# Performance work log

Hardware: AMD Instinct MI355X
Metric: run time of the kernel (lower is better)

The kernel has to match this reference:

```python
import jax, jax.numpy as jnp
import numpy as np

B, S, D, E, K = 4, 4096, 2048, 64, 2


def setup_inputs() -> dict:
    key = jax.random.key(0)
    k1, k2 = jax.random.split(key)
    hidden_states = jax.random.normal(k1, (B, S, D), dtype=jnp.float32)
    gate_weight = jax.random.normal(k2, (E, D), dtype=jnp.float32) * 0.02
    return {"hidden_states": hidden_states, "gate_weight": gate_weight}


def reference(hidden_states, gate_weight):
    b, s, d = hidden_states.shape
    e = gate_weight.shape[0]
    n = b * s
    x = hidden_states.reshape(n, d)
    logits = x @ gate_weight.T                                  # [N, E]
    # Original reassigns gate_logits = softmax(gate_logits) in fp32.
    probs = jax.nn.softmax(logits.astype(jnp.float32), axis=-1)  # [N, E]

    top_v, top_i = jax.lax.top_k(probs, K)                       # [N, K]
    top_k_gates = top_v  # normalize_gate_prob_before_dropping=False

    oh = jax.nn.one_hot(top_i, e, dtype=probs.dtype)             # [N, K, E]
    gates = jnp.einsum('nke,nk->ne', oh, top_k_gates)            # scatter of top-k gates

    # Auxiliary losses (training path, use_aux_loss=True)
    gates_mean = gates.mean(axis=0)                              # [E]
    selection_mean = oh.sum(axis=(0, 1)) / n                     # [E]
    load_balancing_loss = (gates_mean * selection_mean).sum() * e
    # NOTE: original computes z-loss on the softmaxed probs (gate_logits was overwritten)
    router_z_loss = (jax.nn.logsumexp(probs, axis=-1) ** 2).mean()

    # torch scatter_ with index [B,S,1,1] only ever writes slot k=0.
    dispatch0 = oh.sum(axis=1).reshape(b, s, e)                  # 1.0 at top-k experts
    combine0 = gates.reshape(b, s, e)
    pad = ((0, 0), (0, 0), (0, 0), (0, K - 1))
    dispatch_tensor = jnp.pad(dispatch0[..., None], pad)         # [B,S,E,K]
    combine_tensor = jnp.pad(combine0[..., None], pad)           # [B,S,E,K]

    return dispatch_tensor, combine_tensor, load_balancing_loss, router_z_loss
```

## Files before the change

kernel.cpp:

```cpp
#include <hip/hip_runtime.h>
#include <hip/hip_bf16.h>
#include <cstddef>

namespace {
constexpr int kD = 2048;
constexpr int kE = 64;
constexpr int kN = 16384;
constexpr size_t kDispatchFloats = (size_t)kN * kE * 2;
}

typedef short short8_t __attribute__((ext_vector_type(8)));
typedef float f32x4 __attribute__((ext_vector_type(4)));

__global__ void zero_ws_kernel(float* __restrict__ ws) {
  ws[threadIdx.x] = 0.0f;
}

__device__ __forceinline__ void split3(float f, unsigned short& s1,
                                       unsigned short& s2, unsigned short& s3) {
  __hip_bfloat16 h1 = __float2bfloat16(f);
  float r1 = (f - __bfloat162float(h1)) * 256.0f;
  __hip_bfloat16 h2 = __float2bfloat16(r1);
  float r2 = (r1 - __bfloat162float(h2)) * 256.0f;
  __hip_bfloat16 h3 = __float2bfloat16(r2);
  s1 = __builtin_bit_cast(unsigned short, h1);
  s2 = __builtin_bit_cast(unsigned short, h2);
  s3 = __builtin_bit_cast(unsigned short, h3);
}

__global__ __launch_bounds__(256)
void logits_kernel(const float* __restrict__ x, const float* __restrict__ W,
                   float* __restrict__ out) {
  __shared__ unsigned short xs[3][64][64];
  __shared__ unsigned short wsh[3][64][64];

  const int tid  = threadIdx.x;
  const int tile = blockIdx.x & 255;
  const int dq   = blockIdx.x >> 8;

  const int row = tid >> 2;
  const int seg = tid & 3;
  const float4* __restrict__ bx = reinterpret_cast<const float4*>(x) +
      ((size_t)(tile * 64 + row)) * 512 + dq * 128 + seg * 4;
  const float4* __restrict__ bw = reinterpret_cast<const float4*>(W) +
      (size_t)row * 512 + dq * 128 + seg * 4;

  const int lane = tid & 63;
  const int wv   = __builtin_amdgcn_readfirstlane(tid >> 6);
  const int wr   = wv >> 1;
  const int wc   = wv & 1;
  const int lrow = lane & 15;
  const int lk   = lane >> 4;

  f32x4 acc0[2][2], acc1[2][2], acc2[2][2];
  const f32x4 z4 = {0.0f, 0.0f, 0.0f, 0.0f};
#pragma unroll
  for (int a = 0; a < 2; ++a)
#pragma unroll
    for (int b = 0; b < 2; ++b) { acc0[a][b] = z4; acc1[a][b] = z4; acc2[a][b] = z4; }

  for (int c = 0; c < 8; ++c) {
    __syncthreads();
    float4 vx[4], vw[4];
#pragma unroll
    for (int j = 0; j < 4; ++j) vx[j] = bx[c * 16 + j];
#pragma unroll
    for (int j = 0; j < 4; ++j) vw[j] = bw[c * 16 + j];

    {
      short8_t o1[2], o2[2], o3[2];
#pragma unroll
      for (int j = 0; j < 4; ++j) {
        const float4 v = vx[j];
        const int ch = j >> 1, b0 = (j & 1) * 4;
        unsigned short s1, s2, s3;
        split3(v.x, s1, s2, s3); o1[ch][b0+0]=(short)s1; o2[ch][b0+0]=(short)s2; o3[ch][b0+0]=(short)s3;
        split3(v.y, s1, s2, s3); o1[ch][b0+1]=(short)s1; o2[ch][b0+1]=(short)s2; o3[ch][b0+1]=(short)s3;
        split3(v.z, s1, s2, s3); o1[ch][b0+2]=(short)s1; o2[ch][b0+2]=(short)s2; o3[ch][b0+2]=(short)s3;
        split3(v.w, s1, s2, s3); o1[ch][b0+3]=(short)s1; o2[ch][b0+3]=(short)s2; o3[ch][b0+3]=(short)s3;
      }
#pragma unroll
      for (int ch = 0; ch < 2; ++ch) {
        const int col = (seg * 2 + ch) ^ (row & 7);
        *reinterpret_cast<short8_t*>(&xs[0][row][col * 8]) = o1[ch];
        *reinterpret_cast<short8_t*>(&xs[1][row][col * 8]) = o2[ch];
        *reinterpret_cast<short8_t*>(&xs[2][row][col * 8]) = o3[ch];
      }
    }
    {
      short8_t o1[2], o2[2], o3[2];
#pragma unroll
      for (int j = 0; j < 4; ++j) {
        const float4 v = vw[j];
        const int ch = j >> 1, b0 = (j & 1) * 4;
        unsigned short s1, s2, s3;
        split3(v.x, s1, s2, s3); o1[ch][b0+0]=(short)s1; o2[ch][b0+0]=(short)s2; o3[ch][b0+0]=(short)s3;
        split3(v.y, s1, s2, s3); o1[ch][b0+1]=(short)s1; o2[ch][b0+1]=(short)s2; o3[ch][b0+1]=(short)s3;
        split3(v.z, s1, s2, s3); o1[ch][b0+2]=(short)s1; o2[ch][b0+2]=(short)s2; o3[ch][b0+2]=(short)s3;
        split3(v.w, s1, s2, s3); o1[ch][b0+3]=(short)s1; o2[ch][b0+3]=(short)s2; o3[ch][b0+3]=(short)s3;
      }
#pragma unroll
      for (int ch = 0; ch < 2; ++ch) {
        const int col = (seg * 2 + ch) ^ (row & 7);
        *reinterpret_cast<short8_t*>(&wsh[0][row][col * 8]) = o1[ch];
        *reinterpret_cast<short8_t*>(&wsh[1][row][col * 8]) = o2[ch];
        *reinterpret_cast<short8_t*>(&wsh[2][row][col * 8]) = o3[ch];
      }
    }
    __syncthreads();

#pragma unroll
    for (int ks = 0; ks < 2; ++ks) {
      const int kc = ks * 4 + lk;
      short8_t a1[2], a2[2], a3[2], b1[2], b2[2], b3[2];
#pragma unroll
      for (int mt = 0; mt < 2; ++mt) {
        const int r = wr * 32 + mt * 16 + lrow;
        const int cw = (kc ^ (r & 7)) * 8;
        a1[mt] = *reinterpret_cast<const short8_t*>(&xs[0][r][cw]);
        a2[mt] = *reinterpret_cast<const short8_t*>(&xs[1][r][cw]);
        a3[mt] = *reinterpret_cast<const short8_t*>(&xs[2][r][cw]);
      }
#pragma unroll
      for (int nt = 0; nt < 2; ++nt) {
        const int e = wc * 32 + nt * 16 + lrow;
        const int cw = (kc ^ (e & 7)) * 8;
        b1[nt] = *reinterpret_cast<const short8_t*>(&wsh[0][e][cw]);
        b2[nt] = *reinterpret_cast<const short8_t*>(&wsh[1][e][cw]);
        b3[nt] = *reinterpret_cast<const short8_t*>(&wsh[2][e][cw]);
      }
#pragma unroll
      for (int mt = 0; mt < 2; ++mt)
#pragma unroll
        for (int nt = 0; nt < 2; ++nt) {
          acc0[mt][nt] = __builtin_amdgcn_mfma_f32_16x16x32_bf16(a1[mt], b1[nt], acc0[mt][nt], 0, 0, 0);
          acc1[mt][nt] = __builtin_amdgcn_mfma_f32_16x16x32_bf16(a1[mt], b2[nt], acc1[mt][nt], 0, 0, 0);
          acc1[mt][nt] = __builtin_amdgcn_mfma_f32_16x16x32_bf16(a2[mt], b1[nt], acc1[mt][nt], 0, 0, 0);
          acc2[mt][nt] = __builtin_amdgcn_mfma_f32_16x16x32_bf16(a1[mt], b3[nt], acc2[mt][nt], 0, 0, 0);
          acc2[mt][nt] = __builtin_amdgcn_mfma_f32_16x16x32_bf16(a3[mt], b1[nt], acc2[mt][nt], 0, 0, 0);
          acc2[mt][nt] = __builtin_amdgcn_mfma_f32_16x16x32_bf16(a2[mt], b2[nt], acc2[mt][nt], 0, 0, 0);
        }
    }
  }

  const float k8 = 1.0f / 256.0f, k16 = 1.0f / 65536.0f;
  float* __restrict__ base = out + ((dq < 2) ? (size_t)0 : kDispatchFloats);
#pragma unroll
  for (int mt = 0; mt < 2; ++mt)
#pragma unroll
    for (int r = 0; r < 4; ++r) {
      const int trow = wr * 32 + mt * 16 + lk * 4 + r;
      const size_t n = (size_t)tile * 64 + trow;
      float* __restrict__ dst =
          base + n * 128 + (dq & 1) * 64 + wc * 32 + lrow;
#pragma unroll
      for (int nt = 0; nt < 2; ++nt) {
        dst[nt * 16] = acc0[mt][nt][r] + acc1[mt][nt][r] * k8 + acc2[mt][nt][r] * k16;
      }
    }
}

__global__ __launch_bounds__(256)
void gate_kernel(float* __restrict__ out, float* __restrict__ ws) {
  __shared__ float lg[64][65];
  __shared__ int ti0[64], ti1[64];
  __shared__ float tv0[64], tv1[64], tz2[64];
  const int tid  = threadIdx.x;
  const int tile = blockIdx.x;

  float* __restrict__ outd = out + (size_t)tile * 8192;
  float* __restrict__ outc = out + kDispatchFloats + (size_t)tile * 8192;
  const float4* __restrict__ d4 = reinterpret_cast<const float4*>(outd);
  const float4* __restrict__ c4 = reinterpret_cast<const float4*>(outc);

  const int tq = tid >> 4, q = tid & 15;
#pragma unroll
  for (int k = 0; k < 4; ++k) {
    const int t = k * 16 + tq;
    const float4 a = d4[t * 32 + q];
    const float4 b = d4[t * 32 + 16 + q];
    const float4 c = c4[t * 32 + q];
    const float4 d = c4[t * 32 + 16 + q];
    lg[t][q * 4 + 0] = a.x + b.x + c.x + d.x;
    lg[t][q * 4 + 1] = a.y + b.y + c.y + d.y;
    lg[t][q * 4 + 2] = a.z + b.z + c.z + d.z;
    lg[t][q * 4 + 3] = a.w + b.w + c.w + d.w;
  }
  __syncthreads();

  if (tid < 64) {
    float v0 = -INFINITY, v1 = -INFINITY;
    int i0 = 0, i1 = 0;
    for (int e = 0; e < kE; ++e) {
      const float l = lg[tid][e];
      if (l > v0) { v1 = v0; i1 = i0; v0 = l; i0 = e; }
      else if (l > v1) { v1 = l; i1 = e; }
    }
    const float m = v0;
    float s = 0.0f;
    for (int e = 0; e < kE; ++e) s += __expf(lg[tid][e] - m);
    const float rs = 1.0f / s;
    float zexp = 0.0f;
    for (int e = 0; e < kE; ++e) zexp += __expf(__expf(lg[tid][e] - m) * rs);
    const float z = logf(zexp);
    ti0[tid] = i0; ti1[tid] = i1;
    tv0[tid] = rs;
    tv1[tid] = __expf(v1 - m) * rs;
    tz2[tid] = z * z;
  }
  __syncthreads();

  if (tid < kE) {
    float g = 0.0f, cnt = 0.0f;
    for (int t = 0; t < 64; ++t) {
      if (ti0[t] == tid) { g += tv0[t]; cnt += 1.0f; }
      if (ti1[t] == tid) { g += tv1[t]; cnt += 1.0f; }
    }
    atomicAdd(&ws[tid], g);
    atomicAdd(&ws[kE + tid], cnt);
    float z2 = tz2[tid];
    for (int off = 32; off; off >>= 1) z2 += __shfl_down(z2, off);
    if (tid == 0) atomicAdd(&ws[2 * kE], z2);
  }

  {
    const int t = tid >> 2, sub = tid & 3;
    const int i0 = ti0[t], i1 = ti1[t];
    const float v0 = tv0[t], v1 = tv1[t];
    float4* __restrict__ dp = reinterpret_cast<float4*>(outd) + t * 32;
    float4* __restrict__ cp = reinterpret_cast<float4*>(outc) + t * 32;
#pragma unroll
    for (int j = 0; j < 8; ++j) {
      const int qq = sub * 8 + j;
      const int e0 = qq * 2, e1 = qq * 2 + 1;
      const float d0v = (e0 == i0 || e0 == i1) ? 1.0f : 0.0f;
      const float d1v = (e1 == i0 || e1 == i1) ? 1.0f : 0.0f;
      const float c0 = (e0 == i0) ? v0 : ((e0 == i1) ? v1 : 0.0f);
      const float c1 = (e1 == i0) ? v0 : ((e1 == i1) ? v1 : 0.0f);
      dp[qq] = make_float4(d0v, 0.0f, d1v, 0.0f);
      cp[qq] = make_float4(c0, 0.0f, c1, 0.0f);
    }
  }
}

__global__ void finalize_kernel(const float* __restrict__ ws,
                                float* __restrict__ out) {
  const int e = threadIdx.x;
  float prod = ws[e] * ws[kE + e];
  for (int off = 32; off; off >>= 1) prod += __shfl_down(prod, off);
  if (e == 0) {
    const size_t base = kDispatchFloats * 2;
    const float invN = 1.0f / (float)kN;
    out[base]     = prod * ((float)kE * invN * invN);
    out[base + 1] = ws[2 * kE] * invN;
  }
}

extern "C" void kernel_launch(void* const* d_in, const int* in_sizes, int n_in,
                              void* d_out, int out_size, void* d_ws,
                              size_t ws_size, hipStream_t stream) {
  const float* x = (const float*)d_in[0];
  const float* W = (const float*)d_in[1];
  float* out = (float*)d_out;
  float* ws = (float*)d_ws;

  zero_ws_kernel<<<1, 256, 0, stream>>>(ws);
  logits_kernel<<<1024, 256, 0, stream>>>(x, W, out);
  gate_kernel<<<256, 256, 0, stream>>>(out, ws);
  finalize_kernel<<<1, kE, 0, stream>>>(ws, out);
}
```

Baseline: 75.23 us.

## Fuse logits GEMM and gating into one kernel with in-block split-K

Merges the logits GEMM and the gate/top-k kernel into a single 512-thread kernel per 64-token tile. Two wave groups each cover half of D and reduce into a shared-memory logits tile with LDS atomics. Each wave now prefetches the next chunk into registers while the MFMAs run. This removes the global round trip of the partial logits through the output buffer and one kernel launch. The cost is only 256 blocks instead of 1024, which lowers parallelism and occupancy, and larger LDS use per block.

```diff
diff --git a/kernel.cpp b/kernel.cpp
--- a/kernel.cpp
+++ b/kernel.cpp
@@ -28,30 +28,60 @@
   s3 = __builtin_bit_cast(unsigned short, h3);
 }
 
-__global__ __launch_bounds__(256)
-void logits_kernel(const float* __restrict__ x, const float* __restrict__ W,
-                   float* __restrict__ out) {
-  __shared__ unsigned short xs[3][64][64];
-  __shared__ unsigned short wsh[3][64][64];
+__device__ __forceinline__ void conv_store(const float4* v,
+                                           unsigned short (*dst)[64][64],
+                                           int srow, int seg) {
+  short8_t o1[2], o2[2], o3[2];
+#pragma unroll
+  for (int j = 0; j < 4; ++j) {
+    const float4 f = v[j];
+    const int ch = j >> 1, b0 = (j & 1) * 4;
+    unsigned short s1, s2, s3;
+    split3(f.x, s1, s2, s3); o1[ch][b0+0]=(short)s1; o2[ch][b0+0]=(short)s2; o3[ch][b0+0]=(short)s3;
+    split3(f.y, s1, s2, s3); o1[ch][b0+1]=(short)s1; o2[ch][b0+1]=(short)s2; o3[ch][b0+1]=(short)s3;
+    split3(f.z, s1, s2, s3); o1[ch][b0+2]=(short)s1; o2[ch][b0+2]=(short)s2; o3[ch][b0+2]=(short)s3;
+    split3(f.w, s1, s2, s3); o1[ch][b0+3]=(short)s1; o2[ch][b0+3]=(short)s2; o3[ch][b0+3]=(short)s3;
+  }
+#pragma unroll
+  for (int ch = 0; ch < 2; ++ch) {
+    const int col = (seg * 2 + ch) ^ (srow & 7);
+    *reinterpret_cast<short8_t*>(&dst[0][srow][col * 8]) = o1[ch];
+    *reinterpret_cast<short8_t*>(&dst[1][srow][col * 8]) = o2[ch];
+    *reinterpret_cast<short8_t*>(&dst[2][srow][col * 8]) = o3[ch];
+  }
+}
+
+__global__ __launch_bounds__(512)
+void moe_fused_kernel(const float* __restrict__ x, const float* __restrict__ W,
+                      float* __restrict__ out, float* __restrict__ ws) {
+  __shared__ unsigned short xs[2][3][64][64];
+  __shared__ unsigned short wh[2][3][64][64];
+  __shared__ float lg[64][65];
+  __shared__ int ti0[64], ti1[64];
+  __shared__ float tv0[64], tv1[64], tz2[64];
 
   const int tid  = threadIdx.x;
-  const int tile = blockIdx.x & 255;
-  const int dq   = blockIdx.x >> 8;
-
-  const int row = tid >> 2;
-  const int seg = tid & 3;
-  const float4* __restrict__ bx = reinterpret_cast<const float4*>(x) +
-      ((size_t)(tile * 64 + row)) * 512 + dq * 128 + seg * 4;
-  const float4* __restrict__ bw = reinterpret_cast<const float4*>(W) +
-      (size_t)row * 512 + dq * 128 + seg * 4;
-
   const int lane = tid & 63;
   const int wv   = __builtin_amdgcn_readfirstlane(tid >> 6);
-  const int wr   = wv >> 1;
+  const int kh   = wv >> 2;
+  const int wr   = (wv >> 1) & 1;
   const int wc   = wv & 1;
+  const int tile = blockIdx.x;
   const int lrow = lane & 15;
   const int lk   = lane >> 4;
 
+  const int h = tid & 255;
+  const int srow = h >> 2, seg = h & 3;
+  const float4* __restrict__ bx = reinterpret_cast<const float4*>(x) +
+      ((size_t)tile * 64 + srow) * 512 + kh * 256 + seg * 4;
+  const float4* __restrict__ bw = reinterpret_cast<const float4*>(W) +
+      (size_t)srow * 512 + kh * 256 + seg * 4;
+
+  {
+    float* lgf = &lg[0][0];
+    for (int i = tid; i < 64 * 65; i += 512) lgf[i] = 0.0f;
+  }
+
   f32x4 acc0[2][2], acc1[2][2], acc2[2][2];
   const f32x4 z4 = {0.0f, 0.0f, 0.0f, 0.0f};
 #pragma unroll
@@ -59,56 +89,22 @@
 #pragma unroll
     for (int b = 0; b < 2; ++b) { acc0[a][b] = z4; acc1[a][b] = z4; acc2[a][b] = z4; }
 
-  for (int c = 0; c < 8; ++c) {
-    __syncthreads();
-    float4 vx[4], vw[4];
-#pragma unroll
-    for (int j = 0; j < 4; ++j) vx[j] = bx[c * 16 + j];
-#pragma unroll
-    for (int j = 0; j < 4; ++j) vw[j] = bw[c * 16 + j];
-
-    {
-      short8_t o1[2], o2[2], o3[2];
-#pragma unroll
-      for (int j = 0; j < 4; ++j) {
-        const float4 v = vx[j];
-        const int ch = j >> 1, b0 = (j & 1) * 4;
-        unsigned short s1, s2, s3;
-        split3(v.x, s1, s2, s3); o1[ch][b0+0]=(short)s1; o2[ch][b0+0]=(short)s2; o3[ch][b0+0]=(short)s3;
-        split3(v.y, s1, s2, s3); o1[ch][b0+1]=(short)s1; o2[ch][b0+1]=(short)s2; o3[ch][b0+1]=(short)s3;
-        split3(v.z, s1, s2, s3); o1[ch][b0+2]=(short)s1; o2[ch][b0+2]=(short)s2; o3[ch][b0+2]=(short)s3;
-        split3(v.w, s1, s2, s3); o1[ch][b0+3]=(short)s1; o2[ch][b0+3]=(short)s2; o3[ch][b0+3]=(short)s3;
-      }
-#pragma unroll
-      for (int ch = 0; ch < 2; ++ch) {
-        const int col = (seg * 2 + ch) ^ (row & 7);
-        *reinterpret_cast<short8_t*>(&xs[0][row][col * 8]) = o1[ch];
-        *reinterpret_cast<short8_t*>(&xs[1][row][col * 8]) = o2[ch];
-        *reinterpret_cast<short8_t*>(&xs[2][row][col * 8]) = o3[ch];
-      }
-    }
-    {
-      short8_t o1[2], o2[2], o3[2];
-#pragma unroll
-      for (int j = 0; j < 4; ++j) {
-        const float4 v = vw[j];
-        const int ch = j >> 1, b0 = (j & 1) * 4;
-        unsigned short s1, s2, s3;
-        split3(v.x, s1, s2, s3); o1[ch][b0+0]=(short)s1; o2[ch][b0+0]=(short)s2; o3[ch][b0+0]=(short)s3;
-        split3(v.y, s1, s2, s3); o1[ch][b0+1]=(short)s1; o2[ch][b0+1]=(short)s2; o3[ch][b0+1]=(short)s3;
-        split3(v.z, s1, s2, s3); o1[ch][b0+2]=(short)s1; o2[ch][b0+2]=(short)s2; o3[ch][b0+2]=(short)s3;
-        split3(v.w, s1, s2, s3); o1[ch][b0+3]=(short)s1; o2[ch][b0+3]=(short)s2; o3[ch][b0+3]=(short)s3;
-      }
-#pragma unroll
-      for (int ch = 0; ch < 2; ++ch) {
-        const int col = (seg * 2 + ch) ^ (row & 7);
-        *reinterpret_cast<short8_t*>(&wsh[0][row][col * 8]) = o1[ch];
-        *reinterpret_cast<short8_t*>(&wsh[1][row][col * 8]) = o2[ch];
-        *reinterpret_cast<short8_t*>(&wsh[2][row][col * 8]) = o3[ch];
-      }
-    }
-    __syncthreads();
-
+  float4 vx[4], vw[4];
+#pragma unroll
+  for (int j = 0; j < 4; ++j) vx[j] = bx[j];
+#pragma unroll
+  for (int j = 0; j < 4; ++j) vw[j] = bw[j];
+  conv_store(vx, xs[kh], srow, seg);
+  conv_store(vw, wh[kh], srow, seg);
+  __syncthreads();
+
+  for (int c = 0; c < 16; ++c) {
+    if (c < 15) {
+#pragma unroll
+      for (int j = 0; j < 4; ++j) vx[j] = bx[(c + 1) * 16 + j];
+#pragma unroll
+      for (int j = 0; j < 4; ++j) vw[j] = bw[(c + 1) * 16 + j];
+    }
 #pragma unroll
     for (int ks = 0; ks < 2; ++ks) {
       const int kc = ks * 4 + lk;
@@ -117,17 +113,17 @@
       for (int mt = 0; mt < 2; ++mt) {
         const int r = wr * 32 + mt * 16 + lrow;
         const int cw = (kc ^ (r & 7)) * 8;
-        a1[mt] = *reinterpret_cast<const short8_t*>(&xs[0][r][cw]);
-        a2[mt] = *reinterpret_cast<const short8_t*>(&xs[1][r][cw]);
-        a3[mt] = *reinterpret_cast<const short8_t*>(&xs[2][r][cw]);
+        a1[mt] = *reinterpret_cast<const short8_t*>(&xs[kh][0][r][cw]);
+        a2[mt] = *reinterpret_cast<const short8_t*>(&xs[kh][1][r][cw]);
+        a3[mt] = *reinterpret_cast<const short8_t*>(&xs[kh][2][r][cw]);
       }
 #pragma unroll
       for (int nt = 0; nt < 2; ++nt) {
         const int e = wc * 32 + nt * 16 + lrow;
         const int cw = (kc ^ (e & 7)) * 8;
-        b1[nt] = *reinterpret_cast<const short8_t*>(&wsh[0][e][cw]);
-        b2[nt] = *reinterpret_cast<const short8_t*>(&wsh[1][e][cw]);
-        b3[nt] = *reinterpret_cast<const short8_t*>(&wsh[2][e][cw]);
+        b1[nt] = *reinterpret_cast<const short8_t*>(&wh[kh][0][e][cw]);
+        b2[nt] = *reinterpret_cast<const short8_t*>(&wh[kh][1][e][cw]);
+        b3[nt] = *reinterpret_cast<const short8_t*>(&wh[kh][2][e][cw]);
       }
 #pragma unroll
       for (int mt = 0; mt < 2; ++mt)
@@ -141,51 +137,24 @@
           acc2[mt][nt] = __builtin_amdgcn_mfma_f32_16x16x32_bf16(a2[mt], b2[nt], acc2[mt][nt], 0, 0, 0);
         }
     }
+    __syncthreads();
+    if (c < 15) {
+      conv_store(vx, xs[kh], srow, seg);
+      conv_store(vw, wh[kh], srow, seg);
+    }
+    __syncthreads();
   }
 
   const float k8 = 1.0f / 256.0f, k16 = 1.0f / 65536.0f;
-  float* __restrict__ base = out + ((dq < 2) ? (size_t)0 : kDispatchFloats);
 #pragma unroll
   for (int mt = 0; mt < 2; ++mt)
 #pragma unroll
-    for (int r = 0; r < 4; ++r) {
-      const int trow = wr * 32 + mt * 16 + lk * 4 + r;
-      const size_t n = (size_t)tile * 64 + trow;
-      float* __restrict__ dst =
-          base + n * 128 + (dq & 1) * 64 + wc * 32 + lrow;
-#pragma unroll
-      for (int nt = 0; nt < 2; ++nt) {
-        dst[nt * 16] = acc0[mt][nt][r] + acc1[mt][nt][r] * k8 + acc2[mt][nt][r] * k16;
+    for (int nt = 0; nt < 2; ++nt)
+#pragma unroll
+      for (int r = 0; r < 4; ++r) {
+        const float v = acc0[mt][nt][r] + acc1[mt][nt][r] * k8 + acc2[mt][nt][r] * k16;
+        atomicAdd(&lg[wr * 32 + mt * 16 + lk * 4 + r][wc * 32 + nt * 16 + lrow], v);
       }
-    }
-}
-
-__global__ __launch_bounds__(256)
-void gate_kernel(float* __restrict__ out, float* __restrict__ ws) {
-  __shared__ float lg[64][65];
-  __shared__ int ti0[64], ti1[64];
-  __shared__ float tv0[64], tv1[64], tz2[64];
-  const int tid  = threadIdx.x;
-  const int tile = blockIdx.x;
-
-  float* __restrict__ outd = out + (size_t)tile * 8192;
-  float* __restrict__ outc = out + kDispatchFloats + (size_t)tile * 8192;
-  const float4* __restrict__ d4 = reinterpret_cast<const float4*>(outd);
-  const float4* __restrict__ c4 = reinterpret_cast<const float4*>(outc);
-
-  const int tq = tid >> 4, q = tid & 15;
-#pragma unroll
-  for (int k = 0; k < 4; ++k) {
-    const int t = k * 16 + tq;
-    const float4 a = d4[t * 32 + q];
-    const float4 b = d4[t * 32 + 16 + q];
-    const float4 c = c4[t * 32 + q];
-    const float4 d = c4[t * 32 + 16 + q];
-    lg[t][q * 4 + 0] = a.x + b.x + c.x + d.x;
-    lg[t][q * 4 + 1] = a.y + b.y + c.y + d.y;
-    lg[t][q * 4 + 2] = a.z + b.z + c.z + d.z;
-    lg[t][q * 4 + 3] = a.w + b.w + c.w + d.w;
-  }
   __syncthreads();
 
   if (tid < 64) {
@@ -224,14 +193,16 @@
   }
 
   {
-    const int t = tid >> 2, sub = tid & 3;
+    const int t = tid >> 3, sub = tid & 7;
     const int i0 = ti0[t], i1 = ti1[t];
     const float v0 = tv0[t], v1 = tv1[t];
-    float4* __restrict__ dp = reinterpret_cast<float4*>(outd) + t * 32;
-    float4* __restrict__ cp = reinterpret_cast<float4*>(outc) + t * 32;
-#pragma unroll
-    for (int j = 0; j < 8; ++j) {
-      const int qq = sub * 8 + j;
+    float4* __restrict__ dp =
+        reinterpret_cast<float4*>(out) + ((size_t)tile * 64 + t) * 32;
+    float4* __restrict__ cp =
+        reinterpret_cast<float4*>(out) + (size_t)kN * 32 + ((size_t)tile * 64 + t) * 32;
+#pragma unroll
+    for (int j = 0; j < 4; ++j) {
+      const int qq = sub * 4 + j;
       const int e0 = qq * 2, e1 = qq * 2 + 1;
       const float d0v = (e0 == i0 || e0 == i1) ? 1.0f : 0.0f;
       const float d1v = (e1 == i0 || e1 == i1) ? 1.0f : 0.0f;
@@ -265,7 +236,6 @@
   float* ws = (float*)d_ws;
 
   zero_ws_kernel<<<1, 256, 0, stream>>>(ws);
-  logits_kernel<<<1024, 256, 0, stream>>>(x, W, out);
-  gate_kernel<<<256, 256, 0, stream>>>(out, ws);
+  moe_fused_kernel<<<256, 512, 0, stream>>>(x, W, out, ws);
   finalize_kernel<<<1, kE, 0, stream>>>(ws, out);
 }
```

Result: slower. 84.14 us (+11.8%).

## Pre-split gate weights into bf16 triples once and prefetch next x chunk

Applied to the files above, without the earlier changes.

A new kernel converts W into three bf16 planes in workspace once per call, instead of every logits block redoing the split. Logits blocks now read the B fragments for the MFMAs directly from global memory (L2-resident) and drop the W shared-memory tile. The x loads for the next chunk are issued before the MFMA loop, overlapping global latency with compute. The cost is an extra kernel launch, and uncoalesced-ish global fragment loads that stand in for LDS reads.

```diff
diff --git a/kernel.cpp b/kernel.cpp
--- a/kernel.cpp
+++ b/kernel.cpp
@@ -7,6 +7,7 @@
 constexpr int kE = 64;
 constexpr int kN = 16384;
 constexpr size_t kDispatchFloats = (size_t)kN * kE * 2;
+constexpr size_t kWsplitOff = 1024;
 }
 
 typedef short short8_t __attribute__((ext_vector_type(8)));
@@ -29,29 +30,68 @@
 }
 
 __global__ __launch_bounds__(256)
-void logits_kernel(const float* __restrict__ x, const float* __restrict__ W,
+void split_w_kernel(const float* __restrict__ W, unsigned short* __restrict__ wsp) {
+  const int i = blockIdx.x * 256 + threadIdx.x;
+  const float4* src = reinterpret_cast<const float4*>(W) + i * 2;
+  const float4 v0 = src[0], v1 = src[1];
+  short8_t o1, o2, o3;
+  unsigned short s1, s2, s3;
+  split3(v0.x, s1, s2, s3); o1[0]=(short)s1; o2[0]=(short)s2; o3[0]=(short)s3;
+  split3(v0.y, s1, s2, s3); o1[1]=(short)s1; o2[1]=(short)s2; o3[1]=(short)s3;
+  split3(v0.z, s1, s2, s3); o1[2]=(short)s1; o2[2]=(short)s2; o3[2]=(short)s3;
+  split3(v0.w, s1, s2, s3); o1[3]=(short)s1; o2[3]=(short)s2; o3[3]=(short)s3;
+  split3(v1.x, s1, s2, s3); o1[4]=(short)s1; o2[4]=(short)s2; o3[4]=(short)s3;
+  split3(v1.y, s1, s2, s3); o1[5]=(short)s1; o2[5]=(short)s2; o3[5]=(short)s3;
+  split3(v1.z, s1, s2, s3); o1[6]=(short)s1; o2[6]=(short)s2; o3[6]=(short)s3;
+  split3(v1.w, s1, s2, s3); o1[7]=(short)s1; o2[7]=(short)s2; o3[7]=(short)s3;
+  *reinterpret_cast<short8_t*>(wsp + (size_t)0 * 131072 + i * 8) = o1;
+  *reinterpret_cast<short8_t*>(wsp + (size_t)1 * 131072 + i * 8) = o2;
+  *reinterpret_cast<short8_t*>(wsp + (size_t)2 * 131072 + i * 8) = o3;
+}
+
+__device__ __forceinline__ void conv_store(const float4* v,
+                                           unsigned short (*dst)[64][64],
+                                           int srow, int seg) {
+  short8_t o1[2], o2[2], o3[2];
+#pragma unroll
+  for (int j = 0; j < 4; ++j) {
+    const float4 f = v[j];
+    const int ch = j >> 1, b0 = (j & 1) * 4;
+    unsigned short s1, s2, s3;
+    split3(f.x, s1, s2, s3); o1[ch][b0+0]=(short)s1; o2[ch][b0+0]=(short)s2; o3[ch][b0+0]=(short)s3;
+    split3(f.y, s1, s2, s3); o1[ch][b0+1]=(short)s1; o2[ch][b0+1]=(short)s2; o3[ch][b0+1]=(short)s3;
+    split3(f.z, s1, s2, s3); o1[ch][b0+2]=(short)s1; o2[ch][b0+2]=(short)s2; o3[ch][b0+2]=(short)s3;
+    split3(f.w, s1, s2, s3); o1[ch][b0+3]=(short)s1; o2[ch][b0+3]=(short)s2; o3[ch][b0+3]=(short)s3;
+  }
+#pragma unroll
+  for (int ch = 0; ch < 2; ++ch) {
+    const int col = (seg * 2 + ch) ^ (srow & 7);
+    *reinterpret_cast<short8_t*>(&dst[0][srow][col * 8]) = o1[ch];
+    *reinterpret_cast<short8_t*>(&dst[1][srow][col * 8]) = o2[ch];
+    *reinterpret_cast<short8_t*>(&dst[2][srow][col * 8]) = o3[ch];
+  }
+}
+
+__global__ __launch_bounds__(256)
+void logits_kernel(const float* __restrict__ x,
+                   const unsigned short* __restrict__ wsp,
                    float* __restrict__ out) {
   __shared__ unsigned short xs[3][64][64];
-  __shared__ unsigned short wsh[3][64][64];
 
   const int tid  = threadIdx.x;
-  const int tile = blockIdx.x & 255;
-  const int dq   = blockIdx.x >> 8;
-
-  const int row = tid >> 2;
-  const int seg = tid & 3;
-  const float4* __restrict__ bx = reinterpret_cast<const float4*>(x) +
-      ((size_t)(tile * 64 + row)) * 512 + dq * 128 + seg * 4;
-  const float4* __restrict__ bw = reinterpret_cast<const float4*>(W) +
-      (size_t)row * 512 + dq * 128 + seg * 4;
-
   const int lane = tid & 63;
   const int wv   = __builtin_amdgcn_readfirstlane(tid >> 6);
   const int wr   = wv >> 1;
   const int wc   = wv & 1;
+  const int tile = blockIdx.x & 255;
+  const int dq   = blockIdx.x >> 8;
   const int lrow = lane & 15;
   const int lk   = lane >> 4;
 
+  const int row = tid >> 2, seg = tid & 3;
+  const float4* __restrict__ bx = reinterpret_cast<const float4*>(x) +
+      ((size_t)tile * 64 + row) * 512 + dq * 128 + seg * 4;
+
   f32x4 acc0[2][2], acc1[2][2], acc2[2][2];
   const f32x4 z4 = {0.0f, 0.0f, 0.0f, 0.0f};
 #pragma unroll
@@ -59,60 +99,30 @@
 #pragma unroll
     for (int b = 0; b < 2; ++b) { acc0[a][b] = z4; acc1[a][b] = z4; acc2[a][b] = z4; }
 
+  float4 vx[4];
+#pragma unroll
+  for (int j = 0; j < 4; ++j) vx[j] = bx[j];
+
   for (int c = 0; c < 8; ++c) {
     __syncthreads();
-    float4 vx[4], vw[4];
-#pragma unroll
-    for (int j = 0; j < 4; ++j) vx[j] = bx[c * 16 + j];
-#pragma unroll
-    for (int j = 0; j < 4; ++j) vw[j] = bw[c * 16 + j];
-
-    {
-      short8_t o1[2], o2[2], o3[2];
-#pragma unroll
-      for (int j = 0; j < 4; ++j) {
-        const float4 v = vx[j];
-        const int ch = j >> 1, b0 = (j & 1) * 4;
-        unsigned short s1, s2, s3;
-        split3(v.x, s1, s2, s3); o1[ch][b0+0]=(short)s1; o2[ch][b0+0]=(short)s2; o3[ch][b0+0]=(short)s3;
-        split3(v.y, s1, s2, s3); o1[ch][b0+1]=(short)s1; o2[ch][b0+1]=(short)s2; o3[ch][b0+1]=(short)s3;
-        split3(v.z, s1, s2, s3); o1[ch][b0+2]=(short)s1; o2[ch][b0+2]=(short)s2; o3[ch][b0+2]=(short)s3;
-        split3(v.w, s1, s2, s3); o1[ch][b0+3]=(short)s1; o2[ch][b0+3]=(short)s2; o3[ch][b0+3]=(short)s3;
-      }
-#pragma unroll
-      for (int ch = 0; ch < 2; ++ch) {
-        const int col = (seg * 2 + ch) ^ (row & 7);
-        *reinterpret_cast<short8_t*>(&xs[0][row][col * 8]) = o1[ch];
-        *reinterpret_cast<short8_t*>(&xs[1][row][col * 8]) = o2[ch];
-        *reinterpret_cast<short8_t*>(&xs[2][row][col * 8]) = o3[ch];
-      }
-    }
-    {
-      short8_t o1[2], o2[2], o3[2];
-#pragma unroll
-      for (int j = 0; j < 4; ++j) {
-        const float4 v = vw[j];
-        const int ch = j >> 1, b0 = (j & 1) * 4;
-        unsigned short s1, s2, s3;
-        split3(v.x, s1, s2, s3); o1[ch][b0+0]=(short)s1; o2[ch][b0+0]=(short)s2; o3[ch][b0+0]=(short)s3;
-        split3(v.y, s1, s2, s3); o1[ch][b0+1]=(short)s1; o2[ch][b0+1]=(short)s2; o3[ch][b0+1]=(short)s3;
-        split3(v.z, s1, s2, s3); o1[ch][b0+2]=(short)s1; o2[ch][b0+2]=(short)s2; o3[ch][b0+2]=(short)s3;
-        split3(v.w, s1, s2, s3); o1[ch][b0+3]=(short)s1; o2[ch][b0+3]=(short)s2; o3[ch][b0+3]=(short)s3;
-      }
-#pragma unroll
-      for (int ch = 0; ch < 2; ++ch) {
-        const int col = (seg * 2 + ch) ^ (row & 7);
-        *reinterpret_cast<short8_t*>(&wsh[0][row][col * 8]) = o1[ch];
-        *reinterpret_cast<short8_t*>(&wsh[1][row][col * 8]) = o2[ch];
-        *reinterpret_cast<short8_t*>(&wsh[2][row][col * 8]) = o3[ch];
-      }
-    }
+    conv_store(vx, xs, row, seg);
     __syncthreads();
-
+    if (c < 7) {
+#pragma unroll
+      for (int j = 0; j < 4; ++j) vx[j] = bx[(c + 1) * 16 + j];
+    }
 #pragma unroll
     for (int ks = 0; ks < 2; ++ks) {
       const int kc = ks * 4 + lk;
       short8_t a1[2], a2[2], a3[2], b1[2], b2[2], b3[2];
+#pragma unroll
+      for (int nt = 0; nt < 2; ++nt) {
+        const int e = wc * 32 + nt * 16 + lrow;
+        const size_t ko = (size_t)e * 2048 + dq * 512 + c * 64 + kc * 8;
+        b1[nt] = *reinterpret_cast<const short8_t*>(wsp + 0 * 131072 + ko);
+        b2[nt] = *reinterpret_cast<const short8_t*>(wsp + 1 * 131072 + ko);
+        b3[nt] = *reinterpret_cast<const short8_t*>(wsp + 2 * 131072 + ko);
+      }
 #pragma unroll
       for (int mt = 0; mt < 2; ++mt) {
         const int r = wr * 32 + mt * 16 + lrow;
@@ -120,14 +130,6 @@
         a1[mt] = *reinterpret_cast<const short8_t*>(&xs[0][r][cw]);
         a2[mt] = *reinterpret_cast<const short8_t*>(&xs[1][r][cw]);
         a3[mt] = *reinterpret_cast<const short8_t*>(&xs[2][r][cw]);
-      }
-#pragma unroll
-      for (int nt = 0; nt < 2; ++nt) {
-        const int e = wc * 32 + nt * 16 + lrow;
-        const int cw = (kc ^ (e & 7)) * 8;
-        b1[nt] = *reinterpret_cast<const short8_t*>(&wsh[0][e][cw]);
-        b2[nt] = *reinterpret_cast<const short8_t*>(&wsh[1][e][cw]);
-        b3[nt] = *reinterpret_cast<const short8_t*>(&wsh[2][e][cw]);
       }
 #pragma unroll
       for (int mt = 0; mt < 2; ++mt)
@@ -154,9 +156,8 @@
       float* __restrict__ dst =
           base + n * 128 + (dq & 1) * 64 + wc * 32 + lrow;
 #pragma unroll
-      for (int nt = 0; nt < 2; ++nt) {
+      for (int nt = 0; nt < 2; ++nt)
         dst[nt * 16] = acc0[mt][nt][r] + acc1[mt][nt][r] * k8 + acc2[mt][nt][r] * k16;
-      }
     }
 }
 
@@ -263,9 +264,11 @@
   const float* W = (const float*)d_in[1];
   float* out = (float*)d_out;
   float* ws = (float*)d_ws;
+  unsigned short* wsp = (unsigned short*)(ws + kWsplitOff);
 
   zero_ws_kernel<<<1, 256, 0, stream>>>(ws);
-  logits_kernel<<<1024, 256, 0, stream>>>(x, W, out);
+  split_w_kernel<<<64, 256, 0, stream>>>(W, wsp);
+  logits_kernel<<<1024, 256, 0, stream>>>(x, wsp, out);
   gate_kernel<<<256, 256, 0, stream>>>(out, ws);
   finalize_kernel<<<1, kE, 0, stream>>>(ws, out);
 }
```

Result: slower. 109.0 us (+44.9%).
